# Kernel optimization log

Hardware: AMD Instinct MI355X
Metric: run time of the kernel (lower is better)

Reference implementation:

```python
import jax, jax.numpy as jnp
import numpy as np

B, T, K, H = 8, 1024, 512, 8


def setup_inputs() -> dict:
    key = jax.random.key(0)
    kx, kq, kk, kv, ko = jax.random.split(key, 5)
    s = 0.02
    return {
        "x": jax.random.normal(kx, (B, T, K), dtype=jnp.float32),
        "Wq": jax.random.normal(kq, (K * H, K), dtype=jnp.float32) * s,
        "Wk": jax.random.normal(kk, (K * H, K), dtype=jnp.float32) * s,
        "Wv": jax.random.normal(kv, (K * H, K), dtype=jnp.float32) * s,
        "Wo": jax.random.normal(ko, (K, K * H), dtype=jnp.float32) * s,
    }


def reference(x, Wq, Wk, Wv, Wo):
    b, t, k = x.shape
    h = H
    scale = k ** 0.25  # applied to both q and k, total 1/sqrt(k)
    # torch Linear: y = x @ W.T ; view (b,t,h,k) then move heads out: (b,h,t,k)
    def proj(W):
        return (x @ W.T).reshape(b, t, h, k).transpose(0, 2, 1, 3)
    q = proj(Wq) / scale
    kk_ = proj(Wk) / scale
    v = proj(Wv)
    dot = jnp.einsum("bhtd,bhsd->bhts", q, kk_)  # (b,h,t,t)
    # causal mask: strict upper triangle (j > i) -> -inf
    causal = jnp.tril(jnp.ones((t, t), dtype=bool))
    dot = jnp.where(causal[None, None], dot, -jnp.inf)
    attn = jax.nn.softmax(dot, axis=-1)
    out = jnp.einsum("bhts,bhsd->bhtd", attn, v)  # (b,h,t,k)
    out = out.transpose(0, 2, 1, 3).reshape(b, t, h * k)
    return out @ Wo.T
```

## Files before the change

### kernel.cpp

```cpp
#include <hip/hip_runtime.h>
#include <hip/hip_bf16.h>
#include <cstdint>
#include <cmath>


typedef __attribute__((ext_vector_type(8))) short short8;
typedef __attribute__((ext_vector_type(4))) float f32x4;

#define DEVINL __device__ __forceinline__

DEVINL float bf2f(ushort u) { union { uint32_t i; float f; } w; w.i = (uint32_t)u << 16; return w.f; }
DEVINL ushort f2bf(float f) {
  union { float f; uint32_t i; } w; w.f = f;
  uint32_t r = w.i + 0x7FFFu + ((w.i >> 16) & 1u);
  return (ushort)(r >> 16);
}

DEVINL void gl_lds16(const ushort* g, ushort* l) {
  __builtin_amdgcn_global_load_lds(
      (const __attribute__((address_space(1))) uint32_t*)g,
      (__attribute__((address_space(3))) uint32_t*)l, 16, 0, 0);
}

__global__ __launch_bounds__(256) void cvt_f32_bf16(const float* __restrict__ in,
                                                    ushort* __restrict__ out,
                                                    int n8, float scale) {
  int i = blockIdx.x * 256 + threadIdx.x;
  if (i >= n8) return;
  const float4* p = (const float4*)in + (size_t)i * 2;
  float4 a = p[0], b = p[1];
  short8 o;
  o[0] = (short)f2bf(a.x * scale); o[1] = (short)f2bf(a.y * scale);
  o[2] = (short)f2bf(a.z * scale); o[3] = (short)f2bf(a.w * scale);
  o[4] = (short)f2bf(b.x * scale); o[5] = (short)f2bf(b.y * scale);
  o[6] = (short)f2bf(b.z * scale); o[7] = (short)f2bf(b.w * scale);
  ((short8*)out)[i] = o;
}

__global__ __launch_bounds__(256) void zerof4(float4* __restrict__ p, int n4) {
  int i = blockIdx.x * 256 + threadIdx.x;
  if (i < n4) p[i] = float4{0.f, 0.f, 0.f, 0.f};
}

template<bool CSKIP, bool CKB, int EPI, bool ZBH>
__global__ __launch_bounds__(256) void gemm_bt(
    const ushort* __restrict__ A0, long long sAb, long long sAh,
    const ushort* __restrict__ B0, long long sBb, long long sBh,
    void* __restrict__ C0, long long sCb, long long sCh,
    int lda, int ldb, int ldc, int K)
{
  const int bm = blockIdx.x, bn = blockIdx.y, bz = blockIdx.z;
  if (CSKIP && bn > bm) return;
  long long za, zb, zc;
  if (ZBH) {
    const long long bi = bz >> 3, hi = bz & 7;
    za = bi * sAb + hi * sAh; zb = bi * sBb + hi * sBh; zc = bi * sCb + hi * sCh;
  } else {
    za = (long long)bz * sAh; zb = (long long)bz * sBh; zc = (long long)bz * sCh;
  }
  const ushort* A = A0 + za;
  const ushort* B = B0 + zb;
  int kend = K;
  if (CKB) { int kb = (bm + 1) * 128; kend = kb < K ? kb : K; }

  __shared__ ushort As[128 * 32];
  __shared__ ushort Bs[128 * 32];

  const int tid = threadIdx.x;
  const int wave = tid >> 6, lane = tid & 63;
  const int wr = wave >> 1, wc = wave & 1;
  const int l15 = lane & 15, kq = lane >> 4;

  const ushort* ag = A + (size_t)(bm * 128 + wave * 16 + (lane >> 2)) * lda + (lane & 3) * 8;
  const ushort* bg = B + (size_t)(bn * 128 + wave * 16 + (lane >> 2)) * ldb + (lane & 3) * 8;
  ushort* al = &As[wave * 16 * 32];
  ushort* bl = &Bs[wave * 16 * 32];
  const size_t aoff = (size_t)64 * lda, boff = (size_t)64 * ldb;

  f32x4 acc[4][4] = {};

  for (int kk = 0; kk < kend; kk += 32) {
    gl_lds16(ag + kk, al);
    gl_lds16(ag + kk + aoff, al + 64 * 32);
    gl_lds16(bg + kk, bl);
    gl_lds16(bg + kk + boff, bl + 64 * 32);
    __syncthreads();

    short8 af[4], bfr[4];
#pragma unroll
    for (int m = 0; m < 4; ++m)
      af[m] = *(const short8*)&As[(wr * 64 + m * 16 + l15) * 32 + kq * 8];
#pragma unroll
    for (int n = 0; n < 4; ++n)
      bfr[n] = *(const short8*)&Bs[(wc * 64 + n * 16 + l15) * 32 + kq * 8];
#pragma unroll
    for (int m = 0; m < 4; ++m)
#pragma unroll
      for (int n = 0; n < 4; ++n)
        acc[m][n] = __builtin_amdgcn_mfma_f32_16x16x32_bf16(af[m], bfr[n], acc[m][n], 0, 0, 0);
    __syncthreads();
  }

  const int r0 = bm * 128 + wr * 64 + (lane >> 4) * 4;
  const int c0 = bn * 128 + wc * 64 + l15;
  if constexpr (EPI == 0) {
    ushort* C = (ushort*)C0 + zc;
#pragma unroll
    for (int m = 0; m < 4; ++m)
#pragma unroll
      for (int n = 0; n < 4; ++n)
#pragma unroll
        for (int r = 0; r < 4; ++r)
          C[(size_t)(r0 + m * 16 + r) * ldc + (c0 + n * 16)] = f2bf(acc[m][n][r]);
  } else if constexpr (EPI == 1) {
    float* C = (float*)C0 + zc;
#pragma unroll
    for (int m = 0; m < 4; ++m)
#pragma unroll
      for (int n = 0; n < 4; ++n)
#pragma unroll
        for (int r = 0; r < 4; ++r)
          C[(size_t)(r0 + m * 16 + r) * ldc + (c0 + n * 16)] = acc[m][n][r];
  } else {
    float* C = (float*)C0 + zc;
#pragma unroll
    for (int m = 0; m < 4; ++m)
#pragma unroll
      for (int n = 0; n < 4; ++n)
#pragma unroll
        for (int r = 0; r < 4; ++r)
          atomicAdd(&C[(size_t)(r0 + m * 16 + r) * ldc + (c0 + n * 16)], acc[m][n][r]);
  }
}

__global__ __launch_bounds__(256) void transposeV(const ushort* __restrict__ QKVg,
                                                  ushort* __restrict__ Vtg) {
  __shared__ ushort tile[64][72];
  const int bx = blockIdx.x;
  const int by = blockIdx.y;
  const int bz = blockIdx.z;
  const int b = bz >> 3, h = bz & 7;
  const int t = threadIdx.x;
  const int r = t >> 2, c = (t & 3) * 16;

  const ushort* src = QKVg + (size_t)(b * 1024 + bx * 64 + r) * 12288 + 8192 + h * 512 + by * 64 + c;
  short8 v0 = *(const short8*)src;
  short8 v1 = *(const short8*)(src + 8);
#pragma unroll
  for (int j = 0; j < 8; ++j) { tile[r][c + j] = (ushort)v0[j]; tile[r][c + 8 + j] = (ushort)v1[j]; }
  __syncthreads();

  ushort* dst = Vtg + (size_t)(bz * 512 + by * 64 + r) * 1024 + bx * 64 + c;
  short8 o0, o1;
#pragma unroll
  for (int j = 0; j < 8; ++j) { o0[j] = (short)tile[c + j][r]; o1[j] = (short)tile[c + 8 + j][r]; }
  *(short8*)dst = o0;
  *(short8*)(dst + 8) = o1;
}

__global__ __launch_bounds__(256) void softmax_causal(ushort* __restrict__ S) {
  const int wave = threadIdx.x >> 6, lane = threadIdx.x & 63;
  const size_t row_id = (size_t)blockIdx.x * 4 + wave;
  const int t = (int)(row_id & 1023);
  ushort* row = S + row_id * 1024;
  const int j0 = lane * 16;

  short8 v0 = *(const short8*)&row[j0];
  short8 v1 = *(const short8*)&row[j0 + 8];
  float f[16];
#pragma unroll
  for (int i = 0; i < 8; ++i) { f[i] = bf2f((ushort)v0[i]); f[8 + i] = bf2f((ushort)v1[i]); }

  float m = -1e30f;
#pragma unroll
  for (int i = 0; i < 16; ++i) {
    if (j0 + i > t) f[i] = -1e30f;
    m = fmaxf(m, f[i]);
  }
#pragma unroll
  for (int off = 32; off; off >>= 1) m = fmaxf(m, __shfl_xor(m, off));

  float s = 0.f;
#pragma unroll
  for (int i = 0; i < 16; ++i) { f[i] = __expf(f[i] - m); s += f[i]; }
#pragma unroll
  for (int off = 32; off; off >>= 1) s += __shfl_xor(s, off);
  const float inv = 1.f / s;

#pragma unroll
  for (int i = 0; i < 8; ++i) {
    v0[i] = (short)f2bf(f[i] * inv);
    v1[i] = (short)f2bf(f[8 + i] * inv);
  }
  *(short8*)&row[j0] = v0;
  *(short8*)&row[j0 + 8] = v1;
}

extern "C" void kernel_launch(void* const* d_in, const int* in_sizes, int n_in,
                              void* d_out, int out_size, void* d_ws, size_t ws_size,
                              hipStream_t stream) {
  const float* x  = (const float*)d_in[0];
  const float* Wq = (const float*)d_in[1];
  const float* Wk = (const float*)d_in[2];
  const float* Wv = (const float*)d_in[3];
  const float* Wo = (const float*)d_in[4];
  float* out = (float*)d_out;

  const int g = (ws_size >= 293601280ull) ? 4 : (ws_size >= 192937984ull) ? 2 : 1;
  const int ng = 8 / g;

  ushort* xb   = (ushort*)d_ws;
  ushort* Wqkv = xb   + (size_t)4194304;
  ushort* Wob  = Wqkv + (size_t)6291456;
  ushort* AO   = Wob  + (size_t)2097152;
  ushort* QKVg = AO   + (size_t)33554432;
  ushort* Vtg  = QKVg + (size_t)g * 12582912;
  ushort* Sg   = Vtg  + (size_t)g * 4194304;

  const float iscale = (float)(1.0 / pow(512.0, 0.25));

  cvt_f32_bf16<<<2048, 256, 0, stream>>>(x,  xb,             524288, 1.0f);
  cvt_f32_bf16<<<1024, 256, 0, stream>>>(Wq, Wqkv,           262144, iscale);
  cvt_f32_bf16<<<1024, 256, 0, stream>>>(Wk, Wqkv + 2097152, 262144, iscale);
  cvt_f32_bf16<<<1024, 256, 0, stream>>>(Wv, Wqkv + 4194304, 262144, 1.0f);
  cvt_f32_bf16<<<1024, 256, 0, stream>>>(Wo, Wob,            262144, 1.0f);

  for (int grp = 0; grp < ng; ++grp) {
    gemm_bt<false, false, 0, false><<<dim3(g * 8, 96, 1), 256, 0, stream>>>(
        xb + (size_t)grp * g * 524288, 0, 0,
        Wqkv, 0, 0,
        QKVg, 0, 0,
        512, 512, 12288, 512);

    transposeV<<<dim3(16, 8, 8 * g), 256, 0, stream>>>(QKVg, Vtg);

    gemm_bt<true, false, 0, true><<<dim3(8, 8, 8 * g), 256, 0, stream>>>(
        QKVg,        12582912LL, 512LL,
        QKVg + 4096, 12582912LL, 512LL,
        Sg,          8388608LL,  1048576LL,
        12288, 12288, 1024, 512);

    softmax_causal<<<g * 2048, 256, 0, stream>>>(Sg);

    gemm_bt<false, true, 0, true><<<dim3(8, 4, 8 * g), 256, 0, stream>>>(
        Sg,  8388608LL, 1048576LL,
        Vtg, 4194304LL, 524288LL,
        AO + (size_t)grp * g * 4194304, 4194304LL, 512LL,
        1024, 1024, 4096, 1024);
  }

  zerof4<<<4096, 256, 0, stream>>>((float4*)out, 1048576);
  gemm_bt<false, false, 2, false><<<dim3(64, 4, 4), 256, 0, stream>>>(
      AO,  0, 1024LL,
      Wob, 0, 1024LL,
      out, 0, 0LL,
      4096, 4096, 512, 1024);
}
```

Baseline: 626.3 us.

## Double-buffer GEMM LDS tiles and stage bf16 epilogue through swizzled LDS

The GEMM main loop now uses two LDS buffers. The next k-tile is prefetched with global_load_lds while the current tile feeds the MFMAs, with explicit vmcnt waits and barriers, so load latency overlaps compute. The bf16 output epilogue writes accumulators into a swizzled LDS tile and then issues coalesced 16-byte row stores instead of scattered 2-byte stores. LDS use doubles, which may lower occupancy. The float-store epilogue variant was dropped.

```diff
diff --git a/kernel.cpp b/kernel.cpp
--- a/kernel.cpp
+++ b/kernel.cpp
@@ -20,6 +20,10 @@
   __builtin_amdgcn_global_load_lds(
       (const __attribute__((address_space(1))) uint32_t*)g,
       (__attribute__((address_space(3))) uint32_t*)l, 16, 0, 0);
+}
+
+DEVINL int csw(int row, int col) {
+  return row * 128 + ((((col >> 4) ^ ((row >> 2) & 7)) << 4) | (col & 15));
 }
 
 __global__ __launch_bounds__(256) void cvt_f32_bf16(const float* __restrict__ in,
@@ -63,8 +67,7 @@
   int kend = K;
   if (CKB) { int kb = (bm + 1) * 128; kend = kb < K ? kb : K; }
 
-  __shared__ ushort As[128 * 32];
-  __shared__ ushort Bs[128 * 32];
+  __shared__ ushort smem[16384];
 
   const int tid = threadIdx.x;
   const int wave = tid >> 6, lane = tid & 63;
@@ -73,19 +76,34 @@
 
   const ushort* ag = A + (size_t)(bm * 128 + wave * 16 + (lane >> 2)) * lda + (lane & 3) * 8;
   const ushort* bg = B + (size_t)(bn * 128 + wave * 16 + (lane >> 2)) * ldb + (lane & 3) * 8;
-  ushort* al = &As[wave * 16 * 32];
-  ushort* bl = &Bs[wave * 16 * 32];
   const size_t aoff = (size_t)64 * lda, boff = (size_t)64 * ldb;
 
-  f32x4 acc[4][4] = {};
-
-  for (int kk = 0; kk < kend; kk += 32) {
+  auto STAGE = [&](int buf, int kk) {
+    ushort* al = &smem[buf * 8192 + wave * 16 * 32];
+    ushort* bl = al + 4096;
     gl_lds16(ag + kk, al);
     gl_lds16(ag + kk + aoff, al + 64 * 32);
     gl_lds16(bg + kk, bl);
     gl_lds16(bg + kk + boff, bl + 64 * 32);
-    __syncthreads();
-
+  };
+
+  f32x4 acc[4][4] = {};
+  const int nt = kend >> 5;
+
+  STAGE(0, 0);
+  for (int t = 0; t < nt; ++t) {
+    const int cur = t & 1;
+    if (t + 1 < nt) {
+      STAGE(cur ^ 1, (t + 1) << 5);
+      asm volatile("s_waitcnt vmcnt(4)" ::: "memory");
+    } else {
+      asm volatile("s_waitcnt vmcnt(0)" ::: "memory");
+    }
+    __builtin_amdgcn_s_barrier();
+    __builtin_amdgcn_sched_barrier(0);
+
+    const ushort* As = &smem[cur * 8192];
+    const ushort* Bs = As + 4096;
     short8 af[4], bfr[4];
 #pragma unroll
     for (int m = 0; m < 4; ++m)
@@ -98,11 +116,11 @@
 #pragma unroll
       for (int n = 0; n < 4; ++n)
         acc[m][n] = __builtin_amdgcn_mfma_f32_16x16x32_bf16(af[m], bfr[n], acc[m][n], 0, 0, 0);
-    __syncthreads();
-  }
-
-  const int r0 = bm * 128 + wr * 64 + (lane >> 4) * 4;
-  const int c0 = bn * 128 + wc * 64 + l15;
+
+    __builtin_amdgcn_s_barrier();
+    __builtin_amdgcn_sched_barrier(0);
+  }
+
   if constexpr (EPI == 0) {
     ushort* C = (ushort*)C0 + zc;
 #pragma unroll
@@ -111,18 +129,19 @@
       for (int n = 0; n < 4; ++n)
 #pragma unroll
         for (int r = 0; r < 4; ++r)
-          C[(size_t)(r0 + m * 16 + r) * ldc + (c0 + n * 16)] = f2bf(acc[m][n][r]);
-  } else if constexpr (EPI == 1) {
-    float* C = (float*)C0 + zc;
-#pragma unroll
-    for (int m = 0; m < 4; ++m)
-#pragma unroll
-      for (int n = 0; n < 4; ++n)
-#pragma unroll
-        for (int r = 0; r < 4; ++r)
-          C[(size_t)(r0 + m * 16 + r) * ldc + (c0 + n * 16)] = acc[m][n][r];
+          smem[csw(wr * 64 + m * 16 + kq * 4 + r, wc * 64 + n * 16 + l15)] = f2bf(acc[m][n][r]);
+    __syncthreads();
+    const int col = (tid & 15) * 8;
+#pragma unroll
+    for (int j = 0; j < 8; ++j) {
+      const int rr = j * 16 + (tid >> 4);
+      *(short8*)&C[(size_t)(bm * 128 + rr) * ldc + bn * 128 + col] =
+          *(const short8*)&smem[csw(rr, col)];
+    }
   } else {
     float* C = (float*)C0 + zc;
+    const int r0 = bm * 128 + wr * 64 + (lane >> 4) * 4;
+    const int c0 = bn * 128 + wc * 64 + l15;
 #pragma unroll
     for (int m = 0; m < 4; ++m)
 #pragma unroll
```

New measurement: 556.8 us. -11.1%, faster.
